# Kernel optimization log

Hardware: AMD Instinct MI355X
Metric: run time of the kernel (lower is better)

The kernel has to match this reference:

```python
import jax, jax.numpy as jnp
import numpy as np

NEG_SLOPE = 0.2  # PyG GATv2Conv default

def gatv2(x, Wl, Wr, a, b):
    # x: [B, N, Fin]; dense fully-connected GATv2, single head.
    xl = x @ Wl                     # source messages  [B, N, D]
    xr = x @ Wr                     # target queries   [B, N, D]
    # e[b, i, j] = a . leaky_relu(xr_i + xl_j)   (GATv2 scoring)
    e = jnp.einsum('bijd,d->bij',
                   jax.nn.leaky_relu(xr[:, :, None, :] + xl[:, None, :, :], NEG_SLOPE),
                   a)                # [B, N, N]
    alpha = jax.nn.softmax(e, axis=2)              # softmax over neighbors j
    return jnp.einsum('bij,bjd->bid', alpha, xl) + b  # [B, N, D]

def branch(x, Wl1, Wr1, a1, b1, Wl2, Wr2, a2, b2):
    h = jnp.tanh(gatv2(x, Wl1, Wr1, a1, b1))
    h = jnp.tanh(gatv2(h, Wl2, Wr2, a2, b2))
    return h.mean(axis=1)           # mean-pool over nodes -> [B, D]

def setup_inputs() -> dict:
    key = jax.random.key(0)
    B, N, F, D = 8, 512, 128, 64
    ks = jax.random.split(key, 17)
    features = jax.random.normal(ks[0], (B, N, F), dtype=jnp.float32)
    def mk(k, fin, fout):
        k1, k2, k3 = jax.random.split(k, 3)
        s = 1.0 / np.sqrt(fin)
        return (jax.random.normal(k1, (fin, fout), jnp.float32) * s,
                jax.random.normal(k2, (fin, fout), jnp.float32) * s,
                jax.random.normal(k3, (fout,), jnp.float32) * (1.0 / np.sqrt(fout)),
                jnp.zeros((fout,), jnp.float32))
    p1_Wl, p1_Wr, p1_a, p1_b = mk(ks[1], F, D)
    p2_Wl, p2_Wr, p2_a, p2_b = mk(ks[2], D, D)
    v1_Wl, v1_Wr, v1_a, v1_b = mk(ks[3], F, D)
    v2_Wl, v2_Wr, v2_a, v2_b = mk(ks[4], D, D)
    return dict(features=features,
                p1_Wl=p1_Wl, p1_Wr=p1_Wr, p1_a=p1_a, p1_b=p1_b,
                p2_Wl=p2_Wl, p2_Wr=p2_Wr, p2_a=p2_a, p2_b=p2_b,
                v1_Wl=v1_Wl, v1_Wr=v1_Wr, v1_a=v1_a, v1_b=v1_b,
                v2_Wl=v2_Wl, v2_Wr=v2_Wr, v2_a=v2_a, v2_b=v2_b)

def reference(features,
              p1_Wl, p1_Wr, p1_a, p1_b, p2_Wl, p2_Wr, p2_a, p2_b,
              v1_Wl, v1_Wr, v1_a, v1_b, v2_Wl, v2_Wr, v2_a, v2_b):
    latent_pi = branch(features, p1_Wl, p1_Wr, p1_a, p1_b, p2_Wl, p2_Wr, p2_a, p2_b)
    latent_vf = branch(features, v1_Wl, v1_Wr, v1_a, v1_b, v2_Wl, v2_Wr, v2_a, v2_b)
    return latent_pi, latent_vf
```

## Files before the change

kernel.cpp:

```cpp
#include <hip/hip_runtime.h>
#include <hip/hip_bf16.h>
#include <math.h>

#define NN 512
#define L2E 1.44269504089f
typedef __attribute__((ext_vector_type(4))) float f32x4;
typedef _Float16 h2v __attribute__((ext_vector_type(2)));
typedef _Float16 h8  __attribute__((ext_vector_type(8)));

#define OFF_XLI  0u
#define OFF_XRH  262144u
#define OFF_VV   524288u
#define OFF_SAH  532480u
#define OFF_XLTF 532608u
#define OFF_H1   794752u
#define OFF_POOL 1319040u

__device__ __forceinline__ float dterm(unsigned xr2, unsigned xl2, unsigned sa2, float acc)
{
#if __has_builtin(__builtin_amdgcn_fdot2)
    h2v z = __builtin_bit_cast(h2v, xr2) + __builtin_bit_cast(h2v, xl2);
    unsigned az = __builtin_bit_cast(unsigned, z) & 0x7FFF7FFFu;
    return __builtin_amdgcn_fdot2(__builtin_bit_cast(h2v, az),
                                  __builtin_bit_cast(h2v, sa2), acc, false);
#else
    h2v z = __builtin_bit_cast(h2v, xr2) + __builtin_bit_cast(h2v, xl2);
    h2v s = __builtin_bit_cast(h2v, sa2);
    acc = fmaf((float)s[0], fabsf((float)z[0]), acc);
    return fmaf((float)s[1], fabsf((float)z[1]), acc);
#endif
}

template<int K>
__global__ __launch_bounds__(256) void kpre(
    const float* __restrict__ src, int srcPerInst,
    const float* __restrict__ Wl0, const float* __restrict__ Wr0, const float* __restrict__ a0,
    const float* __restrict__ Wl1, const float* __restrict__ Wr1, const float* __restrict__ a1,
    float* __restrict__ ws)
{
    __shared__ float xs[16 * K];
    const int rb   = blockIdx.x;
    const int inst = blockIdx.y;
    const int br   = inst >> 3;
    const int tid  = threadIdx.x;
    const int d = tid & 63, ig = tid >> 6;
    const float* Wl = br ? Wl1 : Wl0;
    const float* Wr = br ? Wr1 : Wr0;
    const float* av = br ? a1  : a0;
    const float* sp = src + (size_t)(srcPerInst ? inst : (inst & 7)) * NN * K + (size_t)rb * 16 * K;

    for (int i = tid; i < 4 * K; i += 256) ((float4*)xs)[i] = ((const float4*)sp)[i];
    __syncthreads();

    float accl[4] = {0.f,0.f,0.f,0.f}, accr[4] = {0.f,0.f,0.f,0.f};
#pragma unroll 4
    for (int k4 = 0; k4 < K / 4; ++k4) {
        float xcv[4][4];
#pragma unroll
        for (int rr = 0; rr < 4; ++rr) {
            float4 v = ((const float4*)xs)[(ig * 4 + rr) * (K / 4) + k4];
            xcv[rr][0] = v.x; xcv[rr][1] = v.y; xcv[rr][2] = v.z; xcv[rr][3] = v.w;
        }
#pragma unroll
        for (int e = 0; e < 4; ++e) {
            float wl = Wl[(k4 * 4 + e) * 64 + d];
            float wr = Wr[(k4 * 4 + e) * 64 + d];
#pragma unroll
            for (int rr = 0; rr < 4; ++rr) {
                accl[rr] = fmaf(xcv[rr][e], wl, accl[rr]);
                accr[rr] = fmaf(xcv[rr][e], wr, accr[rr]);
            }
        }
    }

    float aval = av[d];
    unsigned short* XLI  = (unsigned short*)(ws + OFF_XLI);
    unsigned short* XRH  = (unsigned short*)(ws + OFF_XRH);
    unsigned short* SAH  = (unsigned short*)(ws + OFF_SAH);
    unsigned short* XLTF = (unsigned short*)(ws + OFF_XLTF);
    float* VV = ws + OFF_VV;
#pragma unroll
    for (int rr = 0; rr < 4; ++rr) {
        int row = rb * 16 + ig * 4 + rr;
        XRH[(size_t)(inst * NN + row) * 64 + d] =
            __builtin_bit_cast(unsigned short, (_Float16)accr[rr]);
        XLI[((((size_t)inst * 8 + (row >> 6)) * 8 + (d >> 3)) * 64 + (row & 63)) * 8 + (d & 7)] =
            __builtin_bit_cast(unsigned short, (_Float16)accl[rr]);
        XLTF[(size_t)(inst * 64 + d) * NN + row] =
            __builtin_bit_cast(unsigned short, (_Float16)accl[rr]);
        float pv = aval * accl[rr];
#pragma unroll
        for (int mm = 32; mm > 0; mm >>= 1) pv += __shfl_xor(pv, mm, 64);
        if (d == 0) VV[inst * NN + row] = 0.6f * L2E * pv;
    }
    if (rb == 0 && ig == 0 && (inst & 7) == 0)
        SAH[br * 64 + d] = __builtin_bit_cast(unsigned short, (_Float16)(0.4f * L2E * aval));
}

template<int LAYER>
__global__ __launch_bounds__(512, 4) void kattn(
    const float* __restrict__ ws,
    const float* __restrict__ b0, const float* __restrict__ b1,
    float* __restrict__ Hout)
{
    __shared__ unsigned short pbuf[8][1024];
    __shared__ float pout[8][1056];
    __shared__ unsigned short xr_s[16 * 64];
    __shared__ unsigned short sa_s[64];

    const int ib   = blockIdx.x;
    const int inst = blockIdx.y;
    const int br   = inst >> 3;
    const int tid  = threadIdx.x;
    const int lane = tid & 63;
    const int w    = __builtin_amdgcn_readfirstlane(tid >> 6);
    const float* VV = ws + OFF_VV + inst * NN;
    const unsigned short* XLTF = (const unsigned short*)(ws + OFF_XLTF) + (size_t)inst * 64 * NN;
    const float* bias = br ? b1 : b0;

    {
        const unsigned short* XRH = (const unsigned short*)(ws + OFF_XRH) +
                                    ((size_t)inst * NN + ib * 16) * 64;
        if (tid < 128) ((uint4*)xr_s)[tid] = ((const uint4*)XRH)[tid];
        if (tid < 8)
            ((uint4*)sa_s)[tid] = ((const uint4*)((const unsigned short*)(ws + OFF_SAH) + br * 64))[tid];
    }

    unsigned xl2[32];
    {
        const uint4* xli = (const uint4*)(ws + OFF_XLI) + ((size_t)inst * 8 + w) * 8 * 64;
#pragma unroll
        for (int q8 = 0; q8 < 8; ++q8) {
            uint4 v = xli[q8 * 64 + lane];
            xl2[q8*4+0] = v.x; xl2[q8*4+1] = v.y; xl2[q8*4+2] = v.z; xl2[q8*4+3] = v.w;
        }
    }
    float vj = VV[w * 64 + lane];
    __syncthreads();

    float e[16];
#pragma unroll
    for (int ii = 0; ii < 16; ++ii) e[ii] = 0.f;
    const uint4* xr4 = (const uint4*)xr_s;
    const uint4* sa4 = (const uint4*)sa_s;
#pragma unroll
    for (int q8 = 0; q8 < 8; ++q8) {
        uint4 s4 = sa4[q8];
#pragma unroll
        for (int ii = 0; ii < 16; ++ii) {
            uint4 r4 = xr4[ii * 8 + q8];
            float t = dterm(r4.x, xl2[q8*4+0], s4.x, e[ii]);
            t = dterm(r4.y, xl2[q8*4+1], s4.y, t);
            t = dterm(r4.z, xl2[q8*4+2], s4.z, t);
            e[ii] = dterm(r4.w, xl2[q8*4+3], s4.w, t);
        }
    }

    float4 bv[8];
#pragma unroll
    for (int ks = 0; ks < 2; ++ks)
#pragma unroll
        for (int dt = 0; dt < 4; ++dt)
            bv[ks*4+dt] = *(const float4*)&XLTF[(size_t)(dt * 16 + (lane & 15)) * NN +
                                                w * 64 + ks * 32 + (lane >> 4) * 8];

    unsigned short* phw = pbuf[w];
#pragma unroll
    for (int ii = 0; ii < 16; ++ii) {
        float p = exp2f(e[ii] + vj);
        int idx = ii * 64 + (((lane >> 3) ^ (ii & 7)) << 3) + (lane & 7);
        phw[idx] = __builtin_bit_cast(unsigned short, (_Float16)p);
    }

    f32x4 accn[4] = {{0,0,0,0},{0,0,0,0},{0,0,0,0},{0,0,0,0}};
    f32x4 accd = {0, 0, 0, 0};
    const h8 ones = {(_Float16)1.f,(_Float16)1.f,(_Float16)1.f,(_Float16)1.f,
                     (_Float16)1.f,(_Float16)1.f,(_Float16)1.f,(_Float16)1.f};
#pragma unroll
    for (int ks = 0; ks < 2; ++ks) {
        int aidx = (lane & 15) * 64 + ((((ks << 2) + (lane >> 4)) ^ (lane & 7)) << 3);
        h8 a = *(const h8*)&phw[aidx];
#pragma unroll
        for (int dt = 0; dt < 4; ++dt)
            accn[dt] = __builtin_amdgcn_mfma_f32_16x16x32_f16(
                a, __builtin_bit_cast(h8, bv[ks*4+dt]), accn[dt], 0, 0, 0);
        accd = __builtin_amdgcn_mfma_f32_16x16x32_f16(a, ones, accd, 0, 0, 0);
    }

    float* pw = pout[w];
#pragma unroll
    for (int dt = 0; dt < 4; ++dt)
#pragma unroll
        for (int r = 0; r < 4; ++r)
            pw[((lane >> 4) * 4 + r) * 66 + dt * 16 + (lane & 15)] = accn[dt][r];
    if ((lane & 15) == 0) {
#pragma unroll
        for (int r = 0; r < 4; ++r)
            pw[((lane >> 4) * 4 + r) * 66 + 64] = accd[r];
    }
    __syncthreads();

    const int i  = tid >> 5;
    const int dd = tid & 31;
    float s0 = 0.f, s1 = 0.f, dn = 0.f;
#pragma unroll
    for (int ww = 0; ww < 8; ++ww) {
        const float* pb = &pout[ww][i * 66];
        float2 v = *(const float2*)&pb[dd * 2];
        s0 += v.x; s1 += v.y; dn += pb[64];
    }
    float inv = 1.f / dn;
    float v0 = s0 * inv + bias[dd * 2];
    float v1 = s1 * inv + bias[dd * 2 + 1];
    float t0 = 1.f - 2.f / (__expf(2.f * v0) + 1.f);
    float t1 = 1.f - 2.f / (__expf(2.f * v1) + 1.f);

    if (LAYER == 1) {
        *(float2*)&Hout[(size_t)(inst * NN + ib * 16 + i) * 64 + dd * 2] = make_float2(t0, t1);
    } else {
        float s0p = t0 + __shfl_xor(t0, 32, 64);
        float s1p = t1 + __shfl_xor(t1, 32, 64);
        float* poolbuf = (float*)xr_s;
        if (lane < 32) {
            poolbuf[w * 64 + dd * 2]     = s0p;
            poolbuf[w * 64 + dd * 2 + 1] = s1p;
        }
        __syncthreads();
        if (tid < 64) {
            float s = 0.f;
#pragma unroll
            for (int ww = 0; ww < 8; ++ww) s += poolbuf[ww * 64 + tid];
            Hout[((size_t)inst * 32 + ib) * 64 + tid] = s;
        }
    }
}

__global__ __launch_bounds__(64) void kfinal(const float* __restrict__ pool,
                                             float* __restrict__ out)
{
    const int inst = blockIdx.x;
    const int d    = threadIdx.x;
    const float* p = pool + (size_t)inst * 32 * 64 + d;
    float s = 0.f;
#pragma unroll
    for (int ib = 0; ib < 32; ++ib) s += p[ib * 64];
    out[inst * 64 + d] = s * (1.f / NN);
}

extern "C" void kernel_launch(void* const* d_in, const int* in_sizes, int n_in,
                              void* d_out, int out_size, void* d_ws, size_t ws_size,
                              hipStream_t stream)
{
    (void)in_sizes; (void)n_in; (void)out_size; (void)ws_size;
    const float* feat  = (const float*)d_in[0];
    const float* p1_Wl = (const float*)d_in[1],  *p1_Wr = (const float*)d_in[2];
    const float* p1_a  = (const float*)d_in[3],  *p1_b  = (const float*)d_in[4];
    const float* p2_Wl = (const float*)d_in[5],  *p2_Wr = (const float*)d_in[6];
    const float* p2_a  = (const float*)d_in[7],  *p2_b  = (const float*)d_in[8];
    const float* v1_Wl = (const float*)d_in[9],  *v1_Wr = (const float*)d_in[10];
    const float* v1_a  = (const float*)d_in[11], *v1_b  = (const float*)d_in[12];
    const float* v2_Wl = (const float*)d_in[13], *v2_Wr = (const float*)d_in[14];
    const float* v2_a  = (const float*)d_in[15], *v2_b  = (const float*)d_in[16];

    float* ws = (float*)d_ws;
    float* H1 = ws + OFF_H1;
    float* pool = ws + OFF_POOL;
    float* out = (float*)d_out;

    kpre<128><<<dim3(32, 16), 256, 0, stream>>>(feat, 0, p1_Wl, p1_Wr, p1_a,
                                                v1_Wl, v1_Wr, v1_a, ws);
    kattn<1><<<dim3(32, 16), 512, 0, stream>>>(ws, p1_b, v1_b, H1);
    kpre<64><<<dim3(32, 16), 256, 0, stream>>>(H1, 1, p2_Wl, p2_Wr, p2_a,
                                               v2_Wl, v2_Wr, v2_a, ws);
    kattn<2><<<dim3(32, 16), 512, 0, stream>>>(ws, p2_b, v2_b, pool);
    kfinal<<<16, 64, 0, stream>>>(pool, out);
}
```

Baseline: 65.55 us.

## Fuse layer-2 projections into layer-1 attention epilogue, drop second kpre launch

The layer-1 attention kernel now keeps its tanh output tile in shared memory. It computes the layer-2 Wl/Wr projections and the attention-vector dot product directly, writing the fp16 layouts the layer-2 attention kernel consumes. This removes one kernel launch and the round trip of H1 through global memory. Separate workspace buffers hold the layer-2 tensors, and the first kpre also writes the layer-2 scaled attention vector. In exchange, the attention kernel's epilogue gets heavier: each block redoes weight loads from global for only 16 rows, and it uses only 2 rows per wave, which gives low arithmetic reuse.

```diff
diff --git a/kernel.cpp b/kernel.cpp
--- a/kernel.cpp
+++ b/kernel.cpp
@@ -8,13 +8,17 @@
 typedef _Float16 h2v __attribute__((ext_vector_type(2)));
 typedef _Float16 h8  __attribute__((ext_vector_type(8)));
 
-#define OFF_XLI  0u
-#define OFF_XRH  262144u
-#define OFF_VV   524288u
-#define OFF_SAH  532480u
-#define OFF_XLTF 532608u
-#define OFF_H1   794752u
-#define OFF_POOL 1319040u
+#define OFF_XLI1  0u
+#define OFF_XRH1  262144u
+#define OFF_VV1   524288u
+#define OFF_SAH1  532480u
+#define OFF_SAH2  532544u
+#define OFF_XLTF1 532608u
+#define OFF_XLI2  794752u
+#define OFF_XRH2  1056896u
+#define OFF_XLTF2 1319040u
+#define OFF_VV2   1581184u
+#define OFF_POOL  1589376u
 
 __device__ __forceinline__ float dterm(unsigned xr2, unsigned xl2, unsigned sa2, float acc)
 {
@@ -31,23 +35,24 @@
 #endif
 }
 
-template<int K>
 __global__ __launch_bounds__(256) void kpre(
-    const float* __restrict__ src, int srcPerInst,
-    const float* __restrict__ Wl0, const float* __restrict__ Wr0, const float* __restrict__ a0,
-    const float* __restrict__ Wl1, const float* __restrict__ Wr1, const float* __restrict__ a1,
+    const float* __restrict__ src,
+    const float* __restrict__ p1_Wl, const float* __restrict__ p1_Wr, const float* __restrict__ p1_a,
+    const float* __restrict__ v1_Wl, const float* __restrict__ v1_Wr, const float* __restrict__ v1_a,
+    const float* __restrict__ p2_a, const float* __restrict__ v2_a,
     float* __restrict__ ws)
 {
-    __shared__ float xs[16 * K];
+    const int K = 128;
+    __shared__ float xs[16 * 128];
     const int rb   = blockIdx.x;
     const int inst = blockIdx.y;
     const int br   = inst >> 3;
     const int tid  = threadIdx.x;
     const int d = tid & 63, ig = tid >> 6;
-    const float* Wl = br ? Wl1 : Wl0;
-    const float* Wr = br ? Wr1 : Wr0;
-    const float* av = br ? a1  : a0;
-    const float* sp = src + (size_t)(srcPerInst ? inst : (inst & 7)) * NN * K + (size_t)rb * 16 * K;
+    const float* Wl = br ? v1_Wl : p1_Wl;
+    const float* Wr = br ? v1_Wr : p1_Wr;
+    const float* av = br ? v1_a  : p1_a;
+    const float* sp = src + (size_t)(inst & 7) * NN * K + (size_t)rb * 16 * K;
 
     for (int i = tid; i < 4 * K; i += 256) ((float4*)xs)[i] = ((const float4*)sp)[i];
     __syncthreads();
@@ -74,11 +79,12 @@
     }
 
     float aval = av[d];
-    unsigned short* XLI  = (unsigned short*)(ws + OFF_XLI);
-    unsigned short* XRH  = (unsigned short*)(ws + OFF_XRH);
-    unsigned short* SAH  = (unsigned short*)(ws + OFF_SAH);
-    unsigned short* XLTF = (unsigned short*)(ws + OFF_XLTF);
-    float* VV = ws + OFF_VV;
+    unsigned short* XLI  = (unsigned short*)(ws + OFF_XLI1);
+    unsigned short* XRH  = (unsigned short*)(ws + OFF_XRH1);
+    unsigned short* SAH  = (unsigned short*)(ws + OFF_SAH1);
+    unsigned short* SAH2 = (unsigned short*)(ws + OFF_SAH2);
+    unsigned short* XLTF = (unsigned short*)(ws + OFF_XLTF1);
+    float* VV = ws + OFF_VV1;
 #pragma unroll
     for (int rr = 0; rr < 4; ++rr) {
         int row = rb * 16 + ig * 4 + rr;
@@ -93,14 +99,24 @@
         for (int mm = 32; mm > 0; mm >>= 1) pv += __shfl_xor(pv, mm, 64);
         if (d == 0) VV[inst * NN + row] = 0.6f * L2E * pv;
     }
-    if (rb == 0 && ig == 0 && (inst & 7) == 0)
-        SAH[br * 64 + d] = __builtin_bit_cast(unsigned short, (_Float16)(0.4f * L2E * aval));
+    if (rb == 0 && (inst & 7) == 0 && ig == 0) {
+        SAH[br * 64 + d]  = __builtin_bit_cast(unsigned short, (_Float16)(0.4f * L2E * av[d]));
+        SAH2[br * 64 + d] = __builtin_bit_cast(unsigned short,
+                              (_Float16)(0.4f * L2E * (br ? v2_a : p2_a)[d]));
+    }
 }
 
 template<int LAYER>
 __global__ __launch_bounds__(512, 4) void kattn(
-    const float* __restrict__ ws,
+    const unsigned short* __restrict__ XLI, const unsigned short* __restrict__ XRH,
+    const float* __restrict__ VV, const unsigned short* __restrict__ SAH,
+    const unsigned short* __restrict__ XLTF,
     const float* __restrict__ b0, const float* __restrict__ b1,
+    const float* __restrict__ W2l0, const float* __restrict__ W2r0,
+    const float* __restrict__ W2l1, const float* __restrict__ W2r1,
+    const float* __restrict__ a20, const float* __restrict__ a21,
+    unsigned short* __restrict__ XLI2, unsigned short* __restrict__ XRH2,
+    unsigned short* __restrict__ XLTF2, float* __restrict__ VV2,
     float* __restrict__ Hout)
 {
     __shared__ unsigned short pbuf[8][1024];
@@ -114,28 +130,26 @@
     const int tid  = threadIdx.x;
     const int lane = tid & 63;
     const int w    = __builtin_amdgcn_readfirstlane(tid >> 6);
-    const float* VV = ws + OFF_VV + inst * NN;
-    const unsigned short* XLTF = (const unsigned short*)(ws + OFF_XLTF) + (size_t)inst * 64 * NN;
+    const float* VVi = VV + inst * NN;
+    const unsigned short* XLTFi = XLTF + (size_t)inst * 64 * NN;
     const float* bias = br ? b1 : b0;
 
     {
-        const unsigned short* XRH = (const unsigned short*)(ws + OFF_XRH) +
-                                    ((size_t)inst * NN + ib * 16) * 64;
-        if (tid < 128) ((uint4*)xr_s)[tid] = ((const uint4*)XRH)[tid];
-        if (tid < 8)
-            ((uint4*)sa_s)[tid] = ((const uint4*)((const unsigned short*)(ws + OFF_SAH) + br * 64))[tid];
+        const unsigned short* XRHp = XRH + ((size_t)inst * NN + ib * 16) * 64;
+        if (tid < 128) ((uint4*)xr_s)[tid] = ((const uint4*)XRHp)[tid];
+        if (tid < 8) ((uint4*)sa_s)[tid] = ((const uint4*)(SAH + br * 64))[tid];
     }
 
     unsigned xl2[32];
     {
-        const uint4* xli = (const uint4*)(ws + OFF_XLI) + ((size_t)inst * 8 + w) * 8 * 64;
+        const uint4* xli = (const uint4*)XLI + ((size_t)inst * 8 + w) * 512;
 #pragma unroll
         for (int q8 = 0; q8 < 8; ++q8) {
             uint4 v = xli[q8 * 64 + lane];
             xl2[q8*4+0] = v.x; xl2[q8*4+1] = v.y; xl2[q8*4+2] = v.z; xl2[q8*4+3] = v.w;
         }
     }
-    float vj = VV[w * 64 + lane];
+    float vj = VVi[w * 64 + lane];
     __syncthreads();
 
     float e[16];
@@ -161,8 +175,8 @@
     for (int ks = 0; ks < 2; ++ks)
 #pragma unroll
         for (int dt = 0; dt < 4; ++dt)
-            bv[ks*4+dt] = *(const float4*)&XLTF[(size_t)(dt * 16 + (lane & 15)) * NN +
-                                                w * 64 + ks * 32 + (lane >> 4) * 8];
+            bv[ks*4+dt] = *(const float4*)&XLTFi[(size_t)(dt * 16 + (lane & 15)) * NN +
+                                                 w * 64 + ks * 32 + (lane >> 4) * 8];
 
     unsigned short* phw = pbuf[w];
 #pragma unroll
@@ -216,7 +230,52 @@
     float t1 = 1.f - 2.f / (__expf(2.f * v1) + 1.f);
 
     if (LAYER == 1) {
-        *(float2*)&Hout[(size_t)(inst * NN + ib * 16 + i) * 64 + dd * 2] = make_float2(t0, t1);
+        float* h1f = (float*)pbuf;
+        h1f[i * 64 + dd * 2]     = t0;
+        h1f[i * 64 + dd * 2 + 1] = t1;
+        __syncthreads();
+
+        const float* W2l = br ? W2l1 : W2l0;
+        const float* W2r = br ? W2r1 : W2r0;
+        const float* a2  = br ? a21  : a20;
+        const int r0w = w * 2;
+        float accl2[2] = {0.f, 0.f}, accr2[2] = {0.f, 0.f};
+        const float4* h4 = (const float4*)h1f;
+#pragma unroll 4
+        for (int k4 = 0; k4 < 16; ++k4) {
+            float ha[2][4];
+#pragma unroll
+            for (int rr = 0; rr < 2; ++rr) {
+                float4 h = h4[(r0w + rr) * 16 + k4];
+                ha[rr][0] = h.x; ha[rr][1] = h.y; ha[rr][2] = h.z; ha[rr][3] = h.w;
+            }
+#pragma unroll
+            for (int ee = 0; ee < 4; ++ee) {
+                int k = k4 * 4 + ee;
+                float wl = W2l[k * 64 + lane];
+                float wr = W2r[k * 64 + lane];
+#pragma unroll
+                for (int rr = 0; rr < 2; ++rr) {
+                    accl2[rr] = fmaf(ha[rr][ee], wl, accl2[rr]);
+                    accr2[rr] = fmaf(ha[rr][ee], wr, accr2[rr]);
+                }
+            }
+        }
+        float a2v = a2[lane];
+#pragma unroll
+        for (int rr = 0; rr < 2; ++rr) {
+            int row = ib * 16 + r0w + rr;
+            XRH2[(size_t)(inst * NN + row) * 64 + lane] =
+                __builtin_bit_cast(unsigned short, (_Float16)accr2[rr]);
+            XLI2[((((size_t)inst * 8 + (row >> 6)) * 8 + (lane >> 3)) * 64 + (row & 63)) * 8 + (lane & 7)] =
+                __builtin_bit_cast(unsigned short, (_Float16)accl2[rr]);
+            XLTF2[(size_t)(inst * 64 + lane) * NN + row] =
+                __builtin_bit_cast(unsigned short, (_Float16)accl2[rr]);
+            float pv = a2v * accl2[rr];
+#pragma unroll
+            for (int mm = 32; mm > 0; mm >>= 1) pv += __shfl_xor(pv, mm, 64);
+            if (lane == 0) VV2[inst * NN + row] = 0.6f * L2E * pv;
+        }
     } else {
         float s0p = t0 + __shfl_xor(t0, 32, 64);
         float s1p = t1 + __shfl_xor(t1, 32, 64);
@@ -263,15 +322,31 @@
     const float* v2_a  = (const float*)d_in[15], *v2_b  = (const float*)d_in[16];
 
     float* ws = (float*)d_ws;
-    float* H1 = ws + OFF_H1;
+    unsigned short* XLI1  = (unsigned short*)(ws + OFF_XLI1);
+    unsigned short* XRH1  = (unsigned short*)(ws + OFF_XRH1);
+    unsigned short* SAH1  = (unsigned short*)(ws + OFF_SAH1);
+    unsigned short* SAH2  = (unsigned short*)(ws + OFF_SAH2);
+    unsigned short* XLTF1 = (unsigned short*)(ws + OFF_XLTF1);
+    unsigned short* XLI2  = (unsigned short*)(ws + OFF_XLI2);
+    unsigned short* XRH2  = (unsigned short*)(ws + OFF_XRH2);
+    unsigned short* XLTF2 = (unsigned short*)(ws + OFF_XLTF2);
+    float* VV1  = ws + OFF_VV1;
+    float* VV2  = ws + OFF_VV2;
     float* pool = ws + OFF_POOL;
-    float* out = (float*)d_out;
-
-    kpre<128><<<dim3(32, 16), 256, 0, stream>>>(feat, 0, p1_Wl, p1_Wr, p1_a,
-                                                v1_Wl, v1_Wr, v1_a, ws);
-    kattn<1><<<dim3(32, 16), 512, 0, stream>>>(ws, p1_b, v1_b, H1);
-    kpre<64><<<dim3(32, 16), 256, 0, stream>>>(H1, 1, p2_Wl, p2_Wr, p2_a,
-                                               v2_Wl, v2_Wr, v2_a, ws);
-    kattn<2><<<dim3(32, 16), 512, 0, stream>>>(ws, p2_b, v2_b, pool);
+    float* out  = (float*)d_out;
+
+    kpre<<<dim3(32, 16), 256, 0, stream>>>(feat,
+                                           p1_Wl, p1_Wr, p1_a, v1_Wl, v1_Wr, v1_a,
+                                           p2_a, v2_a, ws);
+    kattn<1><<<dim3(32, 16), 512, 0, stream>>>(XLI1, XRH1, VV1, SAH1, XLTF1,
+                                               p1_b, v1_b,
+                                               p2_Wl, p2_Wr, v2_Wl, v2_Wr, p2_a, v2_a,
+                                               XLI2, XRH2, XLTF2, VV2,
+                                               nullptr);
+    kattn<2><<<dim3(32, 16), 512, 0, stream>>>(XLI2, XRH2, VV2, SAH2, XLTF2,
+                                               p2_b, v2_b,
+                                               nullptr, nullptr, nullptr, nullptr, nullptr, nullptr,
+                                               nullptr, nullptr, nullptr, nullptr,
+                                               pool);
     kfinal<<<16, 64, 0, stream>>>(pool, out);
 }
```

Measured after the change: 68.49 us. 4.5% more time.

## Split score tile so each wave reuses xr loads across two j-blocks

Applied to the files above, without the earlier changes.

Each wave now computes an 8-row by two-64-column block of attention scores instead of 16 rows by one 64-column block. Every xr value read from LDS feeds two dot-product chains, which halves LDS reads for xr and gives the compiler two independent accumulation chains to interleave. Each wave also loads twice as many xl registers and writes its probabilities into other waves' pbuf slots. That requires an extra __syncthreads before the MFMA phase and raises register pressure.

```diff
diff --git a/kernel.cpp b/kernel.cpp
--- a/kernel.cpp
+++ b/kernel.cpp
@@ -114,6 +114,10 @@
     const int tid  = threadIdx.x;
     const int lane = tid & 63;
     const int w    = __builtin_amdgcn_readfirstlane(tid >> 6);
+    const int gr   = w >> 2;
+    const int gj   = w & 3;
+    const int jba  = gj * 2;
+    const int jbb  = gj * 2 + 1;
     const float* VV = ws + OFF_VV + inst * NN;
     const unsigned short* XLTF = (const unsigned short*)(ws + OFF_XLTF) + (size_t)inst * 64 * NN;
     const float* bias = br ? b1 : b0;
@@ -126,33 +130,42 @@
             ((uint4*)sa_s)[tid] = ((const uint4*)((const unsigned short*)(ws + OFF_SAH) + br * 64))[tid];
     }
 
-    unsigned xl2[32];
+    unsigned xa[32], xb[32];
     {
-        const uint4* xli = (const uint4*)(ws + OFF_XLI) + ((size_t)inst * 8 + w) * 8 * 64;
+        const uint4* xli = (const uint4*)(ws + OFF_XLI) + (size_t)inst * 8 * 512;
+        const uint4* xla = xli + (size_t)jba * 512;
+        const uint4* xlb = xli + (size_t)jbb * 512;
 #pragma unroll
         for (int q8 = 0; q8 < 8; ++q8) {
-            uint4 v = xli[q8 * 64 + lane];
-            xl2[q8*4+0] = v.x; xl2[q8*4+1] = v.y; xl2[q8*4+2] = v.z; xl2[q8*4+3] = v.w;
-        }
-    }
-    float vj = VV[w * 64 + lane];
-    __syncthreads();
-
-    float e[16];
-#pragma unroll
-    for (int ii = 0; ii < 16; ++ii) e[ii] = 0.f;
+            uint4 va = xla[q8 * 64 + lane];
+            uint4 vb = xlb[q8 * 64 + lane];
+            xa[q8*4+0] = va.x; xa[q8*4+1] = va.y; xa[q8*4+2] = va.z; xa[q8*4+3] = va.w;
+            xb[q8*4+0] = vb.x; xb[q8*4+1] = vb.y; xb[q8*4+2] = vb.z; xb[q8*4+3] = vb.w;
+        }
+    }
+    float vja = VV[jba * 64 + lane];
+    float vjb = VV[jbb * 64 + lane];
+    __syncthreads();
+
+    float ea[8], eb[8];
+#pragma unroll
+    for (int ii = 0; ii < 8; ++ii) { ea[ii] = 0.f; eb[ii] = 0.f; }
     const uint4* xr4 = (const uint4*)xr_s;
     const uint4* sa4 = (const uint4*)sa_s;
 #pragma unroll
     for (int q8 = 0; q8 < 8; ++q8) {
         uint4 s4 = sa4[q8];
 #pragma unroll
-        for (int ii = 0; ii < 16; ++ii) {
-            uint4 r4 = xr4[ii * 8 + q8];
-            float t = dterm(r4.x, xl2[q8*4+0], s4.x, e[ii]);
-            t = dterm(r4.y, xl2[q8*4+1], s4.y, t);
-            t = dterm(r4.z, xl2[q8*4+2], s4.z, t);
-            e[ii] = dterm(r4.w, xl2[q8*4+3], s4.w, t);
+        for (int ii = 0; ii < 8; ++ii) {
+            uint4 r4 = xr4[(gr * 8 + ii) * 8 + q8];
+            float ta = dterm(r4.x, xa[q8*4+0], s4.x, ea[ii]);
+            float tb = dterm(r4.x, xb[q8*4+0], s4.x, eb[ii]);
+            ta = dterm(r4.y, xa[q8*4+1], s4.y, ta);
+            tb = dterm(r4.y, xb[q8*4+1], s4.y, tb);
+            ta = dterm(r4.z, xa[q8*4+2], s4.z, ta);
+            tb = dterm(r4.z, xb[q8*4+2], s4.z, tb);
+            ea[ii] = dterm(r4.w, xa[q8*4+3], s4.w, ta);
+            eb[ii] = dterm(r4.w, xb[q8*4+3], s4.w, tb);
         }
     }
 
@@ -164,14 +177,18 @@
             bv[ks*4+dt] = *(const float4*)&XLTF[(size_t)(dt * 16 + (lane & 15)) * NN +
                                                 w * 64 + ks * 32 + (lane >> 4) * 8];
 
-    unsigned short* phw = pbuf[w];
-#pragma unroll
-    for (int ii = 0; ii < 16; ++ii) {
-        float p = exp2f(e[ii] + vj);
-        int idx = ii * 64 + (((lane >> 3) ^ (ii & 7)) << 3) + (lane & 7);
-        phw[idx] = __builtin_bit_cast(unsigned short, (_Float16)p);
-    }
-
+#pragma unroll
+    for (int ii = 0; ii < 8; ++ii) {
+        int row = gr * 8 + ii;
+        float pa = exp2f(ea[ii] + vja);
+        float pb = exp2f(eb[ii] + vjb);
+        int idx = row * 64 + (((lane >> 3) ^ (row & 7)) << 3) + (lane & 7);
+        pbuf[jba][idx] = __builtin_bit_cast(unsigned short, (_Float16)pa);
+        pbuf[jbb][idx] = __builtin_bit_cast(unsigned short, (_Float16)pb);
+    }
+    __syncthreads();
+
+    const unsigned short* phw = pbuf[w];
     f32x4 accn[4] = {{0,0,0,0},{0,0,0,0},{0,0,0,0},{0,0,0,0}};
     f32x4 accd = {0, 0, 0, 0};
     const h8 ones = {(_Float16)1.f,(_Float16)1.f,(_Float16)1.f,(_Float16)1.f,
```

After: 66.93 us. 2.1% more time.
